# Kernel tuning notes

Hardware: AMD Instinct MI355X
Metric: run time of the kernel (lower is better)

## Reference

```python
import jax, jax.numpy as jnp
import numpy as np

N = 100000
E = 1600000
F_IN, HID, OUT = 64, 64, 32

def setup_inputs() -> dict:
    key = jax.random.key(0)
    ks = jax.random.split(key, 16)
    s = 0.05
    return {
        "x": jax.random.normal(ks[0], (N, F_IN), jnp.float32),
        "edge_index": jax.random.randint(ks[1], (2, E), 0, N, jnp.int64),
        "edge_attr": jax.random.uniform(ks[2], (E, 1), jnp.float32),
        # distance_processor: Linear(1,16) -> ReLU -> Linear(16,1)
        "Wd1": jax.random.normal(ks[3], (1, 16), jnp.float32) * s,
        "bd1": jnp.zeros((16,), jnp.float32),
        "Wd2": jax.random.normal(ks[4], (16, 1), jnp.float32) * s,
        "bd2": jnp.zeros((1,), jnp.float32),
        # conv1 / conv2 GCN linear weights (in, out) + post-aggregation bias
        "W1c": jax.random.normal(ks[5], (F_IN, HID), jnp.float32) * s,
        "b1c": jnp.zeros((HID,), jnp.float32),
        "W2c": jax.random.normal(ks[6], (HID, HID), jnp.float32) * s,
        "b2c": jnp.zeros((HID,), jnp.float32),
        # output head Linear(hidden, output)
        "Wo": jax.random.normal(ks[7], (HID, OUT), jnp.float32) * s,
        "bo": jnp.zeros((OUT,), jnp.float32),
    }


def _gcn_conv(x, src, dst, ew, W, b, n_nodes):
    """PyG GCNConv with edge weights: add self-loops (weight 1), symmetric norm."""
    h = x @ W                                            # [N, out]
    loop = jnp.arange(n_nodes, dtype=src.dtype)
    src_a = jnp.concatenate([src, loop])                 # [E+N]
    dst_a = jnp.concatenate([dst, loop])
    ew_a = jnp.concatenate([ew, jnp.ones((n_nodes,), ew.dtype)])
    deg = jax.ops.segment_sum(ew_a, dst_a, num_segments=n_nodes)
    dinv = jnp.where(deg > 0, jax.lax.rsqrt(jnp.maximum(deg, 1e-30)), 0.0)
    norm = dinv[src_a] * ew_a * dinv[dst_a]              # [E+N]
    msg = norm[:, None] * h[src_a]                       # gather + scale
    agg = jax.ops.segment_sum(msg, dst_a, num_segments=n_nodes)  # scatter-add
    return agg + b


def reference(x, edge_index, edge_attr, Wd1, bd1, Wd2, bd2, W1c, b1c, W2c, b2c, Wo, bo):
    src, dst = edge_index[0], edge_index[1]
    # edge weight from tiny MLP on distance, squeezed to [E]
    hmlp = jax.nn.relu(edge_attr @ Wd1 + bd1)
    ew = jax.nn.sigmoid(hmlp @ Wd2 + bd2)[:, 0]
    h = jax.nn.relu(_gcn_conv(x, src, dst, ew, W1c, b1c, N))
    # dropout is identity in eval mode
    h = _gcn_conv(h, src, dst, ew, W2c, b2c, N)
    return h @ Wo + bo
```

## Files before the change

### kernel.cpp

```cpp
#include <hip/hip_runtime.h>
#include <hip/hip_fp16.h>
#include <math.h>

#define NBMAX 400
#define GBUILD 512

__device__ inline ushort f2bf(float f) {
    unsigned u = __float_as_uint(f);
    u += 0x7fff + ((u >> 16) & 1);
    return (ushort)(u >> 16);
}
__device__ inline float bf2f(ushort u) {
    return __uint_as_float(((unsigned)u) << 16);
}

__global__ __launch_bounds__(256) void k_tobf16(const float4* __restrict__ X4,
                                                ushort4* __restrict__ Y4, int n4) {
    int i = blockIdx.x * 256 + threadIdx.x;
    if (i >= n4) return;
    float4 v = X4[i];
    ushort4 o;
    o.x = f2bf(v.x); o.y = f2bf(v.y); o.z = f2bf(v.z); o.w = f2bf(v.w);
    Y4[i] = o;
}

__global__ __launch_bounds__(256) void k_hist(const int* __restrict__ dstv,
                                              int* __restrict__ bh,
                                              int E, int chunk) {
    __shared__ int lh[NBMAX];
    int tid = threadIdx.x;
    for (int i = tid; i < NBMAX; i += 256) lh[i] = 0;
    __syncthreads();
    int start = blockIdx.x * chunk;
    int end = min(E, start + chunk);
    for (int e = start + tid; e < end; e += 256)
        atomicAdd(&lh[dstv[e] >> 8], 1);
    __syncthreads();
    int* row = bh + (size_t)blockIdx.x * NBMAX;
    for (int i = tid; i < NBMAX; i += 256) row[i] = lh[i];
}

__global__ __launch_bounds__(256) void k_scanA(const int* __restrict__ bh,
                                               int* __restrict__ boff,
                                               int* __restrict__ btot) {
    __shared__ int s[GBUILD];
    int b = blockIdx.x;
    int t = threadIdx.x;
    int i0 = t, i1 = t + 256;
    s[i0] = bh[(size_t)i0 * NBMAX + b];
    s[i1] = bh[(size_t)i1 * NBMAX + b];
    __syncthreads();
    int c0 = s[i0], c1 = s[i1];
    for (int o = 1; o < GBUILD; o <<= 1) {
        int v0 = (i0 >= o) ? s[i0 - o] : 0;
        int v1 = (i1 >= o) ? s[i1 - o] : 0;
        __syncthreads();
        s[i0] += v0;
        s[i1] += v1;
        __syncthreads();
    }
    boff[(size_t)i0 * NBMAX + b] = s[i0] - c0;
    boff[(size_t)i1 * NBMAX + b] = s[i1] - c1;
    if (t == 0) btot[b] = s[GBUILD - 1];
}

__global__ __launch_bounds__(512) void k_scanB(const int* __restrict__ btot,
                                               int* __restrict__ bbase, int nb) {
    __shared__ int s[512];
    int t = threadIdx.x;
    int c = (t < nb) ? btot[t] : 0;
    s[t] = c;
    __syncthreads();
    for (int o = 1; o < 512; o <<= 1) {
        int v = (t >= o) ? s[t - o] : 0;
        __syncthreads();
        s[t] += v;
        __syncthreads();
    }
    if (t < nb) bbase[t] = s[t] - c;
}

__global__ __launch_bounds__(256) void k_edge_scatter(const float* __restrict__ ea,
                                                      const float* __restrict__ Wd1,
                                                      const float* __restrict__ bd1,
                                                      const float* __restrict__ Wd2,
                                                      const float* __restrict__ bd2,
                                                      const int* __restrict__ srcv,
                                                      const int* __restrict__ dstv,
                                                      const int* __restrict__ bbase,
                                                      const int* __restrict__ boff,
                                                      int2* __restrict__ spk,
                                                      int E, int chunk) {
    __shared__ float w1[16], b1[16], w2[16];
    __shared__ float b2s;
    __shared__ int gb[NBMAX], lc[NBMAX];
    int tid = threadIdx.x;
    if (tid < 16) {
        w1[tid] = Wd1[tid];
        b1[tid] = bd1[tid];
        w2[tid] = Wd2[tid];
    }
    if (tid == 0) b2s = bd2[0];
    const int* brow = boff + (size_t)blockIdx.x * NBMAX;
    for (int i = tid; i < NBMAX; i += 256) {
        gb[i] = bbase[i] + brow[i];
        lc[i] = 0;
    }
    __syncthreads();
    int start = blockIdx.x * chunk;
    int end = min(E, start + chunk);
    for (int e = start + tid; e < end; e += 256) {
        float a = ea[e];
        float s = b2s;
#pragma unroll
        for (int j = 0; j < 16; ++j) {
            float h = fmaxf(a * w1[j] + b1[j], 0.0f);
            s += h * w2[j];
        }
        float w = 1.0f / (1.0f + expf(-s));
        int d = dstv[e];
        int b = d >> 8;
        int p = gb[b] + atomicAdd(&lc[b], 1);
        unsigned payload = ((unsigned)(d & 255) << 16) |
                           (unsigned)__half_as_ushort(__float2half(w));
        spk[p] = make_int2(srcv[e], (int)payload);
    }
}

__global__ __launch_bounds__(256) void k_group(const int2* __restrict__ spk,
                                               const int* __restrict__ bbase,
                                               int2* __restrict__ slots,
                                               int* __restrict__ rowst,
                                               int* __restrict__ cntg,
                                               float* __restrict__ dinv,
                                               int nb, int n, int E) {
    __shared__ int cnt[256], sc[256], ls[256], cur[256];
    __shared__ float dsum[256];
    int b = blockIdx.x;
    int tid = threadIdx.x;
    int r0 = bbase[b];
    int r1 = (b + 1 < nb) ? bbase[b + 1] : E;
    cnt[tid] = 0; cur[tid] = 0; dsum[tid] = 0.0f;
    __syncthreads();
    for (int i = r0 + tid; i < r1; i += 256) {
        int2 pr = spk[i];
        int dl = (pr.y >> 16) & 255;
        atomicAdd(&cnt[dl], 1);
        atomicAdd(&dsum[dl], __half2float(__ushort_as_half((ushort)(pr.y & 0xffff))));
    }
    __syncthreads();
    sc[tid] = cnt[tid];
    __syncthreads();
    for (int o = 1; o < 256; o <<= 1) {
        int v = (tid >= o) ? sc[tid - o] : 0;
        __syncthreads();
        sc[tid] += v;
        __syncthreads();
    }
    ls[tid] = sc[tid] - cnt[tid];
    int dst = (b << 8) + tid;
    if (dst < n) {
        rowst[dst] = r0 + ls[tid];
        cntg[dst] = cnt[tid];
        dinv[dst] = 1.0f / sqrtf(1.0f + dsum[tid]);
    }
    __syncthreads();
    for (int i = r0 + tid; i < r1; i += 256) {
        int2 pr = spk[i];
        int dl = (pr.y >> 16) & 255;
        float wf = __half2float(__ushort_as_half((ushort)(pr.y & 0xffff)));
        int p = r0 + ls[dl] + atomicAdd(&cur[dl], 1);
        slots[p] = make_int2(pr.x, __float_as_int(wf));
    }
}

__global__ __launch_bounds__(256) void k_edge2(const float* __restrict__ ea,
                                               const float* __restrict__ Wd1,
                                               const float* __restrict__ bd1,
                                               const float* __restrict__ Wd2,
                                               const float* __restrict__ bd2,
                                               const int* __restrict__ dstv,
                                               float* __restrict__ ew,
                                               int* __restrict__ cnt, int E) {
    __shared__ float w1[16], b1[16], w2[16];
    __shared__ float b2s;
    if (threadIdx.x < 16) {
        w1[threadIdx.x] = Wd1[threadIdx.x];
        b1[threadIdx.x] = bd1[threadIdx.x];
        w2[threadIdx.x] = Wd2[threadIdx.x];
    }
    if (threadIdx.x == 0) b2s = bd2[0];
    __syncthreads();
    int e = blockIdx.x * 256 + threadIdx.x;
    if (e >= E) return;
    float a = ea[e];
    float s = b2s;
#pragma unroll
    for (int j = 0; j < 16; ++j) {
        float h = fmaxf(a * w1[j] + b1[j], 0.0f);
        s += h * w2[j];
    }
    float w = 1.0f / (1.0f + expf(-s));
    ew[e] = w;
    atomicAdd(&cnt[dstv[e]], 1);
}

__global__ __launch_bounds__(256) void k_scan(const int* __restrict__ cnt,
                                              int* __restrict__ rowst,
                                              int* __restrict__ cursor,
                                              int* __restrict__ gcnt, int n) {
    int i = blockIdx.x * 256 + threadIdx.x;
    int lane = threadIdx.x & 63;
    int c = (i < n) ? cnt[i] : 0;
    int pref = c;
#pragma unroll
    for (int o = 1; o < 64; o <<= 1) {
        int t = __shfl_up(pref, o);
        if (lane >= o) pref += t;
    }
    int total = __shfl(pref, 63);
    int base = 0;
    if (lane == 63 && total > 0) base = atomicAdd(gcnt, total);
    base = __shfl(base, 63);
    if (i < n) {
        int start = base + pref - c;
        rowst[i] = start;
        cursor[i] = start;
    }
}

__global__ __launch_bounds__(256) void k_fill2(const int* __restrict__ srcv,
                                               const int* __restrict__ dstv,
                                               const float* __restrict__ ew,
                                               int* __restrict__ cursor,
                                               int2* __restrict__ slots, int E) {
    int e = blockIdx.x * 256 + threadIdx.x;
    if (e >= E) return;
    int p = atomicAdd(&cursor[dstv[e]], 1);
    slots[p] = make_int2(srcv[e], __float_as_int(ew[e]));
}

__global__ __launch_bounds__(256) void k_deg(const int2* __restrict__ slots,
                                             const int* __restrict__ cnt,
                                             const int* __restrict__ rowst,
                                             float* __restrict__ dinv, int n) {
    int t = blockIdx.x * 256 + threadIdx.x;
    int g = t >> 3;
    int sub = t & 7;
    if (g >= n) return;
    int c = cnt[g];
    size_t base = (size_t)rowst[g];
    float s = 0.0f;
    for (int j = sub; j < c; j += 8) s += __int_as_float(slots[base + j].y);
    s += __shfl_xor(s, 1);
    s += __shfl_xor(s, 2);
    s += __shfl_xor(s, 4);
    if (sub == 0) dinv[g] = 1.0f / sqrtf(1.0f + s);
}

__global__ __launch_bounds__(256) void k_agg(const ushort4* __restrict__ Hb,
                                             const int2* __restrict__ slots,
                                             const int* __restrict__ cnt,
                                             const int* __restrict__ rowst,
                                             const float* __restrict__ dinv,
                                             float* __restrict__ Y, int n) {
    float4* Y4 = (float4*)Y;
    int wid = (blockIdx.x * 256 + threadIdx.x) >> 6;
    int lane = threadIdx.x & 63;
    int l = lane & 15;
    int slb = lane & 48;
    int node = wid * 4 + (lane >> 4);
    bool valid = node < n;
    int nc = valid ? node : 0;
    float di = dinv[nc];
    int c = valid ? cnt[nc] : 0;
    size_t base = (size_t)rowst[nc];

    ushort4 h0 = Hb[(size_t)nc * 16 + l];
    float a0 = di * bf2f(h0.x), a1 = di * bf2f(h0.y);
    float a2 = di * bf2f(h0.z), a3 = di * bf2f(h0.w);
    float b0f = 0.f, b1f = 0.f, b2f = 0.f, b3f = 0.f;
    float c0f = 0.f, c1f = 0.f, c2f = 0.f, c3f = 0.f;
    float d0f = 0.f, d1f = 0.f, d2f = 0.f, d3f = 0.f;

    for (int bb = 0; bb < c; bb += 16) {
        int myc = 0;
        float myw = 0.0f;
        if (bb + l < c) {
            int2 pr = slots[base + bb + l];
            myc = pr.x;
            myw = __int_as_float(pr.y) * dinv[myc];
        }
        int mi = min(16, c - bb);
        for (int i = 0; i < mi; i += 4) {
            int n0 = __shfl(myc, slb + i);
            int n1 = __shfl(myc, slb + i + 1);
            int n2 = __shfl(myc, slb + i + 2);
            int n3 = __shfl(myc, slb + i + 3);
            float w0 = __shfl(myw, slb + i);
            float w1 = __shfl(myw, slb + i + 1);
            float w2 = __shfl(myw, slb + i + 2);
            float w3 = __shfl(myw, slb + i + 3);
            ushort4 v0 = Hb[(size_t)n0 * 16 + l];
            ushort4 v1 = Hb[(size_t)n1 * 16 + l];
            ushort4 v2 = Hb[(size_t)n2 * 16 + l];
            ushort4 v3 = Hb[(size_t)n3 * 16 + l];
            a0 += w0 * bf2f(v0.x); a1 += w0 * bf2f(v0.y);
            a2 += w0 * bf2f(v0.z); a3 += w0 * bf2f(v0.w);
            b0f += w1 * bf2f(v1.x); b1f += w1 * bf2f(v1.y);
            b2f += w1 * bf2f(v1.z); b3f += w1 * bf2f(v1.w);
            c0f += w2 * bf2f(v2.x); c1f += w2 * bf2f(v2.y);
            c2f += w2 * bf2f(v2.z); c3f += w2 * bf2f(v2.w);
            d0f += w3 * bf2f(v3.x); d1f += w3 * bf2f(v3.y);
            d2f += w3 * bf2f(v3.z); d3f += w3 * bf2f(v3.w);
        }
    }
    if (valid) {
        float4 o;
        o.x = di * ((a0 + b0f) + (c0f + d0f));
        o.y = di * ((a1 + b1f) + (c1f + d1f));
        o.z = di * ((a2 + b2f) + (c2f + d2f));
        o.w = di * ((a3 + b3f) + (c3f + d3f));
        Y4[(size_t)node * 16 + l] = o;
    }
}

template <int OUTC, bool RELU, bool BF16OUT>
__global__ __launch_bounds__(256) void k_gemm(const float* __restrict__ X,
                                              const float* __restrict__ W,
                                              const float* __restrict__ bias,
                                              void* __restrict__ Yv, int nrows) {
    __shared__ __align__(16) float ws[64 * OUTC];
    __shared__ __align__(16) float xs[64][64];
    int tid = threadIdx.x;
    for (int i = tid; i < 64 * OUTC / 4; i += 256)
        ((float4*)ws)[i] = ((const float4*)W)[i];
    int row0 = blockIdx.x * 64;
    for (int i = tid; i < 64 * 16; i += 256) {
        int r = i >> 4, c4 = i & 15;
        int gr = row0 + r;
        float4 v = make_float4(0.f, 0.f, 0.f, 0.f);
        if (gr < nrows) v = ((const float4*)X)[(size_t)gr * 16 + c4];
        ((float4*)&xs[r][0])[c4] = v;
    }
    __syncthreads();

    int col = tid % OUTC;
    constexpr int RSLOTS = 256 / OUTC;
    constexpr int RPT = 64 / RSLOTS;
    int rs = tid / OUTC;
    float wc[64];
#pragma unroll
    for (int k = 0; k < 64; ++k) wc[k] = ws[k * OUTC + col];
    float bcol = bias[col];

    for (int rr = 0; rr < RPT; ++rr) {
        int r = rs * RPT + rr;
        const float4* x4 = (const float4*)&xs[r][0];
        float acc = 0.0f;
#pragma unroll
        for (int k4 = 0; k4 < 16; ++k4) {
            float4 v = x4[k4];
            acc += v.x * wc[4 * k4 + 0];
            acc += v.y * wc[4 * k4 + 1];
            acc += v.z * wc[4 * k4 + 2];
            acc += v.w * wc[4 * k4 + 3];
        }
        float o = acc + bcol;
        if (RELU) o = fmaxf(o, 0.0f);
        int gr = row0 + r;
        if (gr < nrows) {
            if (BF16OUT) ((ushort*)Yv)[(size_t)gr * OUTC + col] = f2bf(o);
            else         ((float*)Yv)[(size_t)gr * OUTC + col] = o;
        }
    }
}

__global__ __launch_bounds__(256) void k_prepW(const float* __restrict__ W2c,
                                               const float* __restrict__ Wo,
                                               const float* __restrict__ b2c,
                                               const float* __restrict__ bo,
                                               float* __restrict__ W2o,
                                               float* __restrict__ bo2) {
    int t = threadIdx.x;
    for (int idx = t; idx < 64 * 32; idx += 256) {
        int i = idx >> 5, j = idx & 31;
        float s = 0.0f;
        for (int k = 0; k < 64; ++k) s += W2c[i * 64 + k] * Wo[k * 32 + j];
        W2o[idx] = s;
    }
    if (t < 32) {
        float s = bo[t];
        for (int k = 0; k < 64; ++k) s += b2c[k] * Wo[k * 32 + t];
        bo2[t] = s;
    }
}

extern "C" void kernel_launch(void* const* d_in, const int* in_sizes, int n_in,
                              void* d_out, int out_size, void* d_ws, size_t ws_size,
                              hipStream_t stream) {
    const float* x   = (const float*)d_in[0];
    const int*   ei  = (const int*)d_in[1];
    const float* ea  = (const float*)d_in[2];
    const float* Wd1 = (const float*)d_in[3];
    const float* bd1 = (const float*)d_in[4];
    const float* Wd2 = (const float*)d_in[5];
    const float* bd2 = (const float*)d_in[6];
    const float* W1c = (const float*)d_in[7];
    const float* b1c = (const float*)d_in[8];
    const float* W2c = (const float*)d_in[9];
    const float* b2c = (const float*)d_in[10];
    const float* Wo  = (const float*)d_in[11];
    const float* bo  = (const float*)d_in[12];

    const int N = in_sizes[0] / 64;
    const int E = in_sizes[2];
    const int* srcv = ei;
    const int* dstv = ei + E;
    const int NB = (N + 255) >> 8;

    size_t off = 0;
    auto alloc = [&](size_t bytes) -> void* {
        void* p = (char*)d_ws + off;
        off += (bytes + 255) & ~(size_t)255;
        return p;
    };

    int*    cntg  = (int*)   alloc((size_t)N * 4);
    int*    rowst = (int*)   alloc((size_t)N * 4);
    float*  dinv  = (float*) alloc((size_t)N * 4);
    ushort* xb    = (ushort*)alloc((size_t)N * 64 * 2);
    float*  buf1  = (float*) alloc((size_t)N * 64 * 4);
    ushort* buf1b = (ushort*)alloc((size_t)N * 64 * 2);
    float*  W2o   = (float*) alloc(64 * 32 * 4);
    float*  bo2   = (float*) alloc(32 * 4);
    int2*   slots = (int2*)  alloc((size_t)E * 8);
    float*  buf2  = buf1;

    const int BA = (N + 15) / 16;
    const int BG = (N + 63) / 64;
    const int BT = (N * 16 + 255) / 256;
    const int GB = GBUILD;
    const int CHUNK = (E + GB - 1) / GB;

    size_t base_need = off;
    size_t sort_need = base_need + (((size_t)E * 8 + 255) & ~(size_t)255)
                       + 2 * ((size_t)GB * NBMAX * 4 + 256) + 16384;
    const bool fast = ws_size >= sort_need;

    if (fast) {
        int2* spk  = (int2*)alloc((size_t)E * 8);
        int* bh    = (int*) alloc((size_t)GB * NBMAX * 4);
        int* boff  = (int*) alloc((size_t)GB * NBMAX * 4);
        int* btot  = (int*) alloc(NBMAX * 4);
        int* bbase = (int*) alloc(NBMAX * 4);

        k_tobf16<<<BT, 256, 0, stream>>>((const float4*)x, (ushort4*)xb, N * 16);
        k_hist<<<GB, 256, 0, stream>>>(dstv, bh, E, CHUNK);
        k_scanA<<<NBMAX, 256, 0, stream>>>(bh, boff, btot);
        k_scanB<<<1, 512, 0, stream>>>(btot, bbase, NB);
        k_edge_scatter<<<GB, 256, 0, stream>>>(ea, Wd1, bd1, Wd2, bd2, srcv, dstv,
                                               bbase, boff, spk, E, CHUNK);
        k_group<<<NB, 256, 0, stream>>>(spk, bbase, slots, rowst, cntg, dinv,
                                        NB, N, E);
        k_prepW<<<1, 256, 0, stream>>>(W2c, Wo, b2c, bo, W2o, bo2);
        k_agg<<<BA, 256, 0, stream>>>((const ushort4*)xb, slots, cntg, rowst,
                                      dinv, buf1, N);
        k_gemm<64, true, true><<<BG, 256, 0, stream>>>(buf1, W1c, b1c, buf1b, N);
        k_agg<<<BA, 256, 0, stream>>>((const ushort4*)buf1b, slots, cntg, rowst,
                                      dinv, buf2, N);
        k_gemm<32, false, false><<<BG, 256, 0, stream>>>(buf2, W2o, bo2, d_out, N);
    } else {
        float* ew   = (float*)alloc((size_t)E * 4);
        int* cursor = (int*)  alloc((size_t)N * 4);
        int* gcnt   = (int*)  alloc(256);
        const int BN = (N + 255) / 256;
        const int BE = (E + 255) / 256;
        const int BD = (N * 8 + 255) / 256;
        hipMemsetAsync(cntg, 0, (size_t)N * 4, stream);
        hipMemsetAsync(gcnt, 0, 4, stream);
        k_tobf16<<<BT, 256, 0, stream>>>((const float4*)x, (ushort4*)xb, N * 16);
        k_edge2<<<BE, 256, 0, stream>>>(ea, Wd1, bd1, Wd2, bd2, dstv, ew, cntg, E);
        k_scan<<<BN, 256, 0, stream>>>(cntg, rowst, cursor, gcnt, N);
        k_fill2<<<BE, 256, 0, stream>>>(srcv, dstv, ew, cursor, slots, E);
        k_deg<<<BD, 256, 0, stream>>>(slots, cntg, rowst, dinv, N);
        k_prepW<<<1, 256, 0, stream>>>(W2c, Wo, b2c, bo, W2o, bo2);
        k_agg<<<BA, 256, 0, stream>>>((const ushort4*)xb, slots, cntg, rowst,
                                      dinv, buf1, N);
        k_gemm<64, true, true><<<BG, 256, 0, stream>>>(buf1, W1c, b1c, buf1b, N);
        k_agg<<<BA, 256, 0, stream>>>((const ushort4*)buf1b, slots, cntg, rowst,
                                      dinv, buf2, N);
        k_gemm<32, false, false><<<BG, 256, 0, stream>>>(buf2, W2o, bo2, d_out, N);
    }
}
```

Measured before the change: 284.0 us.

## Fuse neighbor aggregation with dense GEMM in one block kernel

Replaces the separate aggregation and GEMM kernels with a single kernel per layer. Each 512-thread block aggregates 64 nodes into shared memory, using 8 lanes per node with 16-byte bf16 loads, then applies the weight matrix in place. This removes the fp32 intermediate write and re-read through global memory plus two launches. In exchange the block is larger and there is a sync barrier between the two phases. The gather is also restructured (8 edges per batch, 8 lanes per node), so a warp's nodes can diverge when their degrees differ.

```diff
diff --git a/kernel.cpp b/kernel.cpp
--- a/kernel.cpp
+++ b/kernel.cpp
@@ -4,6 +4,8 @@
 
 #define NBMAX 400
 #define GBUILD 512
+
+typedef __attribute__((ext_vector_type(8))) ushort us8;
 
 __device__ inline ushort f2bf(float f) {
     unsigned u = __float_as_uint(f);
@@ -174,6 +176,111 @@
     }
 }
 
+template <int OUTC, bool RELU, bool BF16OUT>
+__global__ __launch_bounds__(512) void k_agg_gemm(const ushort* __restrict__ Hb,
+                                                  const int2* __restrict__ slots,
+                                                  const int* __restrict__ cnt,
+                                                  const int* __restrict__ rowst,
+                                                  const float* __restrict__ dinv,
+                                                  const float* __restrict__ W,
+                                                  const float* __restrict__ bias,
+                                                  void* __restrict__ Yv, int n) {
+    __shared__ __align__(16) float xs[64][68];
+    __shared__ __align__(16) float ws_[64 * OUTC];
+    const us8* H8 = (const us8*)Hb;
+    int tid = threadIdx.x;
+    for (int i = tid; i < 64 * OUTC / 4; i += 512)
+        ((float4*)ws_)[i] = ((const float4*)W)[i];
+
+    int lane = tid & 63;
+    int g = lane >> 3;
+    int s = lane & 7;
+    int gbase = lane & 56;
+    int nl = (tid >> 6) * 8 + g;
+    int node = blockIdx.x * 64 + nl;
+    bool valid = node < n;
+    int nc = valid ? node : 0;
+    float di = dinv[nc];
+    int c = valid ? cnt[nc] : 0;
+    size_t base = (size_t)rowst[nc];
+
+    float acc[8];
+    us8 h0 = H8[(size_t)nc * 8 + s];
+#pragma unroll
+    for (int j = 0; j < 8; ++j) acc[j] = di * bf2f(h0[j]);
+
+    for (int bb = 0; bb < c; bb += 8) {
+        int myc = 0;
+        float myw = 0.0f;
+        if (bb + s < c) {
+            int2 pr = slots[base + bb + s];
+            myc = pr.x;
+            myw = __int_as_float(pr.y) * dinv[myc];
+        }
+#pragma unroll
+        for (int i = 0; i < 8; ++i) {
+            int ni = __shfl(myc, gbase + i);
+            float wi = __shfl(myw, gbase + i);
+            us8 v = H8[(size_t)ni * 8 + s];
+#pragma unroll
+            for (int j = 0; j < 8; ++j) acc[j] += wi * bf2f(v[j]);
+        }
+    }
+#pragma unroll
+    for (int j = 0; j < 8; ++j) xs[nl][s * 8 + j] = di * acc[j];
+    __syncthreads();
+
+    int col = tid % OUTC;
+    constexpr int RSLOTS = 512 / OUTC;
+    constexpr int RPT = 64 / RSLOTS;
+    int rs = tid / OUTC;
+    float wc[64];
+#pragma unroll
+    for (int k = 0; k < 64; ++k) wc[k] = ws_[k * OUTC + col];
+    float bcol = bias[col];
+
+    for (int rr = 0; rr < RPT; ++rr) {
+        int r = rs * RPT + rr;
+        const float4* x4 = (const float4*)&xs[r][0];
+        float a = 0.0f;
+#pragma unroll
+        for (int k4 = 0; k4 < 16; ++k4) {
+            float4 v = x4[k4];
+            a += v.x * wc[4 * k4 + 0];
+            a += v.y * wc[4 * k4 + 1];
+            a += v.z * wc[4 * k4 + 2];
+            a += v.w * wc[4 * k4 + 3];
+        }
+        float o = a + bcol;
+        if (RELU) o = fmaxf(o, 0.0f);
+        int gr = blockIdx.x * 64 + r;
+        if (gr < n) {
+            if (BF16OUT) ((ushort*)Yv)[(size_t)gr * OUTC + col] = f2bf(o);
+            else         ((float*)Yv)[(size_t)gr * OUTC + col] = o;
+        }
+    }
+}
+
+__global__ __launch_bounds__(256) void k_prepW(const float* __restrict__ W2c,
+                                               const float* __restrict__ Wo,
+                                               const float* __restrict__ b2c,
+                                               const float* __restrict__ bo,
+                                               float* __restrict__ W2o,
+                                               float* __restrict__ bo2) {
+    int t = threadIdx.x;
+    for (int idx = t; idx < 64 * 32; idx += 256) {
+        int i = idx >> 5, j = idx & 31;
+        float s = 0.0f;
+        for (int k = 0; k < 64; ++k) s += W2c[i * 64 + k] * Wo[k * 32 + j];
+        W2o[idx] = s;
+    }
+    if (t < 32) {
+        float s = bo[t];
+        for (int k = 0; k < 64; ++k) s += b2c[k] * Wo[k * 32 + t];
+        bo2[t] = s;
+    }
+}
+
 __global__ __launch_bounds__(256) void k_edge2(const float* __restrict__ ea,
                                                const float* __restrict__ Wd1,
                                                const float* __restrict__ bd1,
@@ -258,144 +365,6 @@
     if (sub == 0) dinv[g] = 1.0f / sqrtf(1.0f + s);
 }
 
-__global__ __launch_bounds__(256) void k_agg(const ushort4* __restrict__ Hb,
-                                             const int2* __restrict__ slots,
-                                             const int* __restrict__ cnt,
-                                             const int* __restrict__ rowst,
-                                             const float* __restrict__ dinv,
-                                             float* __restrict__ Y, int n) {
-    float4* Y4 = (float4*)Y;
-    int wid = (blockIdx.x * 256 + threadIdx.x) >> 6;
-    int lane = threadIdx.x & 63;
-    int l = lane & 15;
-    int slb = lane & 48;
-    int node = wid * 4 + (lane >> 4);
-    bool valid = node < n;
-    int nc = valid ? node : 0;
-    float di = dinv[nc];
-    int c = valid ? cnt[nc] : 0;
-    size_t base = (size_t)rowst[nc];
-
-    ushort4 h0 = Hb[(size_t)nc * 16 + l];
-    float a0 = di * bf2f(h0.x), a1 = di * bf2f(h0.y);
-    float a2 = di * bf2f(h0.z), a3 = di * bf2f(h0.w);
-    float b0f = 0.f, b1f = 0.f, b2f = 0.f, b3f = 0.f;
-    float c0f = 0.f, c1f = 0.f, c2f = 0.f, c3f = 0.f;
-    float d0f = 0.f, d1f = 0.f, d2f = 0.f, d3f = 0.f;
-
-    for (int bb = 0; bb < c; bb += 16) {
-        int myc = 0;
-        float myw = 0.0f;
-        if (bb + l < c) {
-            int2 pr = slots[base + bb + l];
-            myc = pr.x;
-            myw = __int_as_float(pr.y) * dinv[myc];
-        }
-        int mi = min(16, c - bb);
-        for (int i = 0; i < mi; i += 4) {
-            int n0 = __shfl(myc, slb + i);
-            int n1 = __shfl(myc, slb + i + 1);
-            int n2 = __shfl(myc, slb + i + 2);
-            int n3 = __shfl(myc, slb + i + 3);
-            float w0 = __shfl(myw, slb + i);
-            float w1 = __shfl(myw, slb + i + 1);
-            float w2 = __shfl(myw, slb + i + 2);
-            float w3 = __shfl(myw, slb + i + 3);
-            ushort4 v0 = Hb[(size_t)n0 * 16 + l];
-            ushort4 v1 = Hb[(size_t)n1 * 16 + l];
-            ushort4 v2 = Hb[(size_t)n2 * 16 + l];
-            ushort4 v3 = Hb[(size_t)n3 * 16 + l];
-            a0 += w0 * bf2f(v0.x); a1 += w0 * bf2f(v0.y);
-            a2 += w0 * bf2f(v0.z); a3 += w0 * bf2f(v0.w);
-            b0f += w1 * bf2f(v1.x); b1f += w1 * bf2f(v1.y);
-            b2f += w1 * bf2f(v1.z); b3f += w1 * bf2f(v1.w);
-            c0f += w2 * bf2f(v2.x); c1f += w2 * bf2f(v2.y);
-            c2f += w2 * bf2f(v2.z); c3f += w2 * bf2f(v2.w);
-            d0f += w3 * bf2f(v3.x); d1f += w3 * bf2f(v3.y);
-            d2f += w3 * bf2f(v3.z); d3f += w3 * bf2f(v3.w);
-        }
-    }
-    if (valid) {
-        float4 o;
-        o.x = di * ((a0 + b0f) + (c0f + d0f));
-        o.y = di * ((a1 + b1f) + (c1f + d1f));
-        o.z = di * ((a2 + b2f) + (c2f + d2f));
-        o.w = di * ((a3 + b3f) + (c3f + d3f));
-        Y4[(size_t)node * 16 + l] = o;
-    }
-}
-
-template <int OUTC, bool RELU, bool BF16OUT>
-__global__ __launch_bounds__(256) void k_gemm(const float* __restrict__ X,
-                                              const float* __restrict__ W,
-                                              const float* __restrict__ bias,
-                                              void* __restrict__ Yv, int nrows) {
-    __shared__ __align__(16) float ws[64 * OUTC];
-    __shared__ __align__(16) float xs[64][64];
-    int tid = threadIdx.x;
-    for (int i = tid; i < 64 * OUTC / 4; i += 256)
-        ((float4*)ws)[i] = ((const float4*)W)[i];
-    int row0 = blockIdx.x * 64;
-    for (int i = tid; i < 64 * 16; i += 256) {
-        int r = i >> 4, c4 = i & 15;
-        int gr = row0 + r;
-        float4 v = make_float4(0.f, 0.f, 0.f, 0.f);
-        if (gr < nrows) v = ((const float4*)X)[(size_t)gr * 16 + c4];
-        ((float4*)&xs[r][0])[c4] = v;
-    }
-    __syncthreads();
-
-    int col = tid % OUTC;
-    constexpr int RSLOTS = 256 / OUTC;
-    constexpr int RPT = 64 / RSLOTS;
-    int rs = tid / OUTC;
-    float wc[64];
-#pragma unroll
-    for (int k = 0; k < 64; ++k) wc[k] = ws[k * OUTC + col];
-    float bcol = bias[col];
-
-    for (int rr = 0; rr < RPT; ++rr) {
-        int r = rs * RPT + rr;
-        const float4* x4 = (const float4*)&xs[r][0];
-        float acc = 0.0f;
-#pragma unroll
-        for (int k4 = 0; k4 < 16; ++k4) {
-            float4 v = x4[k4];
-            acc += v.x * wc[4 * k4 + 0];
-            acc += v.y * wc[4 * k4 + 1];
-            acc += v.z * wc[4 * k4 + 2];
-            acc += v.w * wc[4 * k4 + 3];
-        }
-        float o = acc + bcol;
-        if (RELU) o = fmaxf(o, 0.0f);
-        int gr = row0 + r;
-        if (gr < nrows) {
-            if (BF16OUT) ((ushort*)Yv)[(size_t)gr * OUTC + col] = f2bf(o);
-            else         ((float*)Yv)[(size_t)gr * OUTC + col] = o;
-        }
-    }
-}
-
-__global__ __launch_bounds__(256) void k_prepW(const float* __restrict__ W2c,
-                                               const float* __restrict__ Wo,
-                                               const float* __restrict__ b2c,
-                                               const float* __restrict__ bo,
-                                               float* __restrict__ W2o,
-                                               float* __restrict__ bo2) {
-    int t = threadIdx.x;
-    for (int idx = t; idx < 64 * 32; idx += 256) {
-        int i = idx >> 5, j = idx & 31;
-        float s = 0.0f;
-        for (int k = 0; k < 64; ++k) s += W2c[i * 64 + k] * Wo[k * 32 + j];
-        W2o[idx] = s;
-    }
-    if (t < 32) {
-        float s = bo[t];
-        for (int k = 0; k < 64; ++k) s += b2c[k] * Wo[k * 32 + t];
-        bo2[t] = s;
-    }
-}
-
 extern "C" void kernel_launch(void* const* d_in, const int* in_sizes, int n_in,
                               void* d_out, int out_size, void* d_ws, size_t ws_size,
                               hipStream_t stream) {
@@ -430,15 +399,12 @@
     int*    rowst = (int*)   alloc((size_t)N * 4);
     float*  dinv  = (float*) alloc((size_t)N * 4);
     ushort* xb    = (ushort*)alloc((size_t)N * 64 * 2);
-    float*  buf1  = (float*) alloc((size_t)N * 64 * 4);
-    ushort* buf1b = (ushort*)alloc((size_t)N * 64 * 2);
+    ushort* h1b   = (ushort*)alloc((size_t)N * 64 * 2);
     float*  W2o   = (float*) alloc(64 * 32 * 4);
     float*  bo2   = (float*) alloc(32 * 4);
     int2*   slots = (int2*)  alloc((size_t)E * 8);
-    float*  buf2  = buf1;
-
-    const int BA = (N + 15) / 16;
-    const int BG = (N + 63) / 64;
+
+    const int BF = (N + 63) / 64;
     const int BT = (N * 16 + 255) / 256;
     const int GB = GBUILD;
     const int CHUNK = (E + GB - 1) / GB;
@@ -464,12 +430,10 @@
         k_group<<<NB, 256, 0, stream>>>(spk, bbase, slots, rowst, cntg, dinv,
                                         NB, N, E);
         k_prepW<<<1, 256, 0, stream>>>(W2c, Wo, b2c, bo, W2o, bo2);
-        k_agg<<<BA, 256, 0, stream>>>((const ushort4*)xb, slots, cntg, rowst,
-                                      dinv, buf1, N);
-        k_gemm<64, true, true><<<BG, 256, 0, stream>>>(buf1, W1c, b1c, buf1b, N);
-        k_agg<<<BA, 256, 0, stream>>>((const ushort4*)buf1b, slots, cntg, rowst,
-                                      dinv, buf2, N);
-        k_gemm<32, false, false><<<BG, 256, 0, stream>>>(buf2, W2o, bo2, d_out, N);
+        k_agg_gemm<64, true, true><<<BF, 512, 0, stream>>>(
+            xb, slots, cntg, rowst, dinv, W1c, b1c, h1b, N);
+        k_agg_gemm<32, false, false><<<BF, 512, 0, stream>>>(
+            h1b, slots, cntg, rowst, dinv, W2o, bo2, d_out, N);
     } else {
         float* ew   = (float*)alloc((size_t)E * 4);
         int* cursor = (int*)  alloc((size_t)N * 4);
@@ -485,11 +449,9 @@
         k_fill2<<<BE, 256, 0, stream>>>(srcv, dstv, ew, cursor, slots, E);
         k_deg<<<BD, 256, 0, stream>>>(slots, cntg, rowst, dinv, N);
         k_prepW<<<1, 256, 0, stream>>>(W2c, Wo, b2c, bo, W2o, bo2);
-        k_agg<<<BA, 256, 0, stream>>>((const ushort4*)xb, slots, cntg, rowst,
-                                      dinv, buf1, N);
-        k_gemm<64, true, true><<<BG, 256, 0, stream>>>(buf1, W1c, b1c, buf1b, N);
-        k_agg<<<BA, 256, 0, stream>>>((const ushort4*)buf1b, slots, cntg, rowst,
-                                      dinv, buf2, N);
-        k_gemm<32, false, false><<<BG, 256, 0, stream>>>(buf2, W2o, bo2, d_out, N);
-    }
-}
+        k_agg_gemm<64, true, true><<<BF, 512, 0, stream>>>(
+            xb, slots, cntg, rowst, dinv, W1c, b1c, h1b, N);
+        k_agg_gemm<32, false, false><<<BF, 512, 0, stream>>>(
+            h1b, slots, cntg, rowst, dinv, W2o, bo2, d_out, N);
+    }
+}
```

Result: slower. 290.2 us (+2.2%).
